# Kernel optimization log

Measured on AMD Instinct MI355X. Metric: run time of the kernel, lower is better.

## Reference

```python
import jax, jax.numpy as jnp
import numpy as np

INPUT_SIZE = 256
HIDDEN = 64
VOCAB = 8000
B, T = 64, 256


def _lstm_layer(x_seq, W_ih, W_hh, b_ih, b_hh):
    # x_seq: [B, T, D_in]; PyTorch gate order: i, f, g, o
    Bsz = x_seq.shape[0]
    H = W_hh.shape[1]
    # Precompute input projections for all timesteps (one big GEMM)
    x_proj = jnp.einsum('btd,gd->btg', x_seq, W_ih) + b_ih + b_hh  # [B,T,4H]

    def step(carry, xt):
        h, c = carry
        gates = xt + h @ W_hh.T  # [B,4H]
        i, f, g, o = jnp.split(gates, 4, axis=-1)
        i = jax.nn.sigmoid(i)
        f = jax.nn.sigmoid(f)
        g = jnp.tanh(g)
        o = jax.nn.sigmoid(o)
        c = f * c + i * g
        h = o * jnp.tanh(c)
        return (h, c), h

    zeros = jnp.zeros((Bsz, H), x_seq.dtype)
    _, hs = jax.lax.scan(step, (zeros, zeros), jnp.swapaxes(x_proj, 0, 1))
    return jnp.swapaxes(hs, 0, 1)  # [B,T,H]


def setup_inputs() -> dict:
    key = jax.random.key(0)
    ks = jax.random.split(key, 12)
    s0 = 1.0 / np.sqrt(HIDDEN)
    x = jax.random.normal(ks[0], (B, T, INPUT_SIZE), dtype=jnp.float32)
    W_ih0 = jax.random.uniform(ks[1], (4 * HIDDEN, INPUT_SIZE), jnp.float32, -s0, s0)
    W_hh0 = jax.random.uniform(ks[2], (4 * HIDDEN, HIDDEN), jnp.float32, -s0, s0)
    b_ih0 = jax.random.uniform(ks[3], (4 * HIDDEN,), jnp.float32, -s0, s0)
    b_hh0 = jax.random.uniform(ks[4], (4 * HIDDEN,), jnp.float32, -s0, s0)
    W_ih1 = jax.random.uniform(ks[5], (4 * HIDDEN, HIDDEN), jnp.float32, -s0, s0)
    W_hh1 = jax.random.uniform(ks[6], (4 * HIDDEN, HIDDEN), jnp.float32, -s0, s0)
    b_ih1 = jax.random.uniform(ks[7], (4 * HIDDEN,), jnp.float32, -s0, s0)
    b_hh1 = jax.random.uniform(ks[8], (4 * HIDDEN,), jnp.float32, -s0, s0)
    Wl = jax.random.uniform(ks[9], (VOCAB, HIDDEN), jnp.float32, -s0, s0)
    bl = jax.random.uniform(ks[10], (VOCAB,), jnp.float32, -s0, s0)
    return {"x": x, "W_ih0": W_ih0, "W_hh0": W_hh0, "b_ih0": b_ih0, "b_hh0": b_hh0,
            "W_ih1": W_ih1, "W_hh1": W_hh1, "b_ih1": b_ih1, "b_hh1": b_hh1,
            "Wl": Wl, "bl": bl}


def reference(x, W_ih0, W_hh0, b_ih0, b_hh0, W_ih1, W_hh1, b_ih1, b_hh1, Wl, bl):
    h1 = _lstm_layer(x, W_ih0, W_hh0, b_ih0, b_hh0)   # [B,T,H]
    h2 = _lstm_layer(h1, W_ih1, W_hh1, b_ih1, b_hh1)  # [B,T,H]
    return jnp.einsum('bth,vh->btv', h2, Wl) + bl      # [B,T,VOCAB]
```

## Files before the change

### kernel.cpp

```cpp
#include <hip/hip_runtime.h>
#include <math.h>

#define HID 64
#define G4 256
#define TSTEPS 256
#define BATCH 64
#define MTOT 16384
#define NVOCAB 8000

__device__ __forceinline__ float tanh_s(float x){
    float ax = fabsf(x);
    float e = __expf(-2.0f*ax);
    float t = (1.0f - e)/(1.0f + e);
    return x >= 0.f ? t : -t;
}

__global__ void transpose_k(const float* __restrict__ src, float* __restrict__ dst, int R, int C){
    int idx = blockIdx.x*256 + threadIdx.x;
    if (idx < R*C){
        int c = idx / R;
        int r = idx - c*R;
        dst[idx] = src[r*C + c];
    }
}

__global__ void bsum_k(const float* __restrict__ a, const float* __restrict__ b, float* __restrict__ o, int n){
    int i = blockIdx.x*256 + threadIdx.x;
    if (i < n) o[i] = a[i] + b[i];
}

template<int KTOT>
__global__ __launch_bounds__(256) void gemm_bias(
    const float* __restrict__ A, const float* __restrict__ Bt,
    const float* __restrict__ bias, float* __restrict__ C,
    int M, int N)
{
    __shared__ float As[128][65];
    __shared__ float Bs[64][128];
    const int tid = threadIdx.x;
    const int tx = tid & 15;
    const int ty = tid >> 4;
    const int m0 = blockIdx.y * 128;
    const int n0 = blockIdx.x * 128;

    float4 acc0[8], acc1[8];
    #pragma unroll
    for (int i = 0; i < 8; i++){
        acc0[i] = make_float4(0.f,0.f,0.f,0.f);
        acc1[i] = make_float4(0.f,0.f,0.f,0.f);
    }

    for (int k0 = 0; k0 < KTOT; k0 += 64){
        {
            const int mi_b = tid >> 4;
            const int k4   = (tid & 15) * 4;
            #pragma unroll
            for (int it = 0; it < 8; it++){
                int mi = it*16 + mi_b;
                float4 v = *(const float4*)(A + (size_t)(m0+mi)*KTOT + k0 + k4);
                As[mi][k4+0] = v.x; As[mi][k4+1] = v.y;
                As[mi][k4+2] = v.z; As[mi][k4+3] = v.w;
            }
        }
        {
            const int ki_b = tid >> 5;
            const int vj   = (tid & 31) * 4;
            #pragma unroll
            for (int it = 0; it < 8; it++){
                int ki = it*8 + ki_b;
                float4 v = make_float4(0.f,0.f,0.f,0.f);
                if (n0 + vj < N)
                    v = *(const float4*)(Bt + (size_t)(k0+ki)*N + n0 + vj);
                *(float4*)&Bs[ki][vj] = v;
            }
        }
        __syncthreads();

        #pragma unroll 8
        for (int k = 0; k < 64; k++){
            float4 b0 = *(const float4*)&Bs[k][tx*4];
            float4 b1 = *(const float4*)&Bs[k][64 + tx*4];
            #pragma unroll
            for (int i = 0; i < 8; i++){
                float av = As[ty*8+i][k];
                acc0[i].x = fmaf(av, b0.x, acc0[i].x);
                acc0[i].y = fmaf(av, b0.y, acc0[i].y);
                acc0[i].z = fmaf(av, b0.z, acc0[i].z);
                acc0[i].w = fmaf(av, b0.w, acc0[i].w);
                acc1[i].x = fmaf(av, b1.x, acc1[i].x);
                acc1[i].y = fmaf(av, b1.y, acc1[i].y);
                acc1[i].z = fmaf(av, b1.z, acc1[i].z);
                acc1[i].w = fmaf(av, b1.w, acc1[i].w);
            }
        }
        __syncthreads();
    }

    const int v0a = n0 + tx*4;
    const int v0b = n0 + 64 + tx*4;
    float4 ba = make_float4(0.f,0.f,0.f,0.f);
    float4 bb = make_float4(0.f,0.f,0.f,0.f);
    if (v0a < N) ba = *(const float4*)(bias + v0a);
    if (v0b < N) bb = *(const float4*)(bias + v0b);
    #pragma unroll
    for (int i = 0; i < 8; i++){
        int m = m0 + ty*8 + i;
        float* crow = C + (size_t)m*N;
        if (v0a < N){
            float4 r;
            r.x = acc0[i].x + ba.x; r.y = acc0[i].y + ba.y;
            r.z = acc0[i].z + ba.z; r.w = acc0[i].w + ba.w;
            *(float4*)(crow + v0a) = r;
        }
        if (v0b < N){
            float4 r;
            r.x = acc1[i].x + bb.x; r.y = acc1[i].y + bb.y;
            r.z = acc1[i].z + bb.z; r.w = acc1[i].w + bb.w;
            *(float4*)(crow + v0b) = r;
        }
    }
}

__global__ __launch_bounds__(256) void lstm_recur(
    const float* __restrict__ XP, const float* __restrict__ Whh,
    float* __restrict__ Hout)
{
    const int b = blockIdx.x;
    const int tid = threadIdx.x;
    __shared__ float4 hsh[16];
    __shared__ float gsh[256];

    float4 w[16];
    const float4* wr = (const float4*)(Whh + (size_t)tid*HID);
    #pragma unroll
    for (int i = 0; i < 16; i++) w[i] = wr[i];

    float c = 0.f;
    if (tid < 64) ((float*)hsh)[tid] = 0.f;
    __syncthreads();

    const float* xprow = XP + (size_t)b*TSTEPS*G4 + tid;
    const bool is_tanh = (tid >= 128) && (tid < 192);
    float xn = xprow[0];

    for (int t = 0; t < TSTEPS; t++){
        float a = xn;
        if (t+1 < TSTEPS) xn = xprow[(size_t)(t+1)*G4];

        float s0=0.f, s1=0.f, s2=0.f, s3=0.f;
        #pragma unroll
        for (int i = 0; i < 16; i += 4){
            float4 h0 = hsh[i+0];
            float4 h1 = hsh[i+1];
            float4 h2 = hsh[i+2];
            float4 h3 = hsh[i+3];
            s0 = fmaf(w[i+0].x,h0.x,s0); s0 = fmaf(w[i+0].y,h0.y,s0);
            s0 = fmaf(w[i+0].z,h0.z,s0); s0 = fmaf(w[i+0].w,h0.w,s0);
            s1 = fmaf(w[i+1].x,h1.x,s1); s1 = fmaf(w[i+1].y,h1.y,s1);
            s1 = fmaf(w[i+1].z,h1.z,s1); s1 = fmaf(w[i+1].w,h1.w,s1);
            s2 = fmaf(w[i+2].x,h2.x,s2); s2 = fmaf(w[i+2].y,h2.y,s2);
            s2 = fmaf(w[i+2].z,h2.z,s2); s2 = fmaf(w[i+2].w,h2.w,s2);
            s3 = fmaf(w[i+3].x,h3.x,s3); s3 = fmaf(w[i+3].y,h3.y,s3);
            s3 = fmaf(w[i+3].z,h3.z,s3); s3 = fmaf(w[i+3].w,h3.w,s3);
        }
        a += (s0+s1) + (s2+s3);

        float aa = is_tanh ? 2.f*a : a;
        float sg = 1.f/(1.f + __expf(-aa));
        float act = is_tanh ? 2.f*sg - 1.f : sg;
        gsh[tid] = act;
        __syncthreads();

        if (tid < 64){
            float ig = gsh[tid];
            float fg = gsh[64+tid];
            float gg = gsh[128+tid];
            float og = gsh[192+tid];
            c = fmaf(fg, c, ig*gg);
            float hn = og * tanh_s(c);
            ((float*)hsh)[tid] = hn;
            Hout[((size_t)b*TSTEPS + t)*HID + tid] = hn;
        }
        __syncthreads();
    }
}

extern "C" void kernel_launch(void* const* d_in, const int* in_sizes, int n_in,
                              void* d_out, int out_size, void* d_ws, size_t ws_size,
                              hipStream_t stream)
{
    const float* x    = (const float*)d_in[0];
    const float* Wih0 = (const float*)d_in[1];
    const float* Whh0 = (const float*)d_in[2];
    const float* bih0 = (const float*)d_in[3];
    const float* bhh0 = (const float*)d_in[4];
    const float* Wih1 = (const float*)d_in[5];
    const float* Whh1 = (const float*)d_in[6];
    const float* bih1 = (const float*)d_in[7];
    const float* bhh1 = (const float*)d_in[8];
    const float* Wl   = (const float*)d_in[9];
    const float* bl   = (const float*)d_in[10];
    float* out = (float*)d_out;

    float* ws  = (float*)d_ws;
    float* Wt0 = ws;
    float* Wt1 = Wt0 + 65536;
    float* WlT = Wt1 + 16384;
    float* bs0 = WlT + 512000;
    float* bs1 = bs0 + 256;
    float* xp0 = bs1 + 256;
    float* xp1 = xp0 + 4194304;
    float* h1  = xp1 + 4194304;
    float* h2  = h1  + 1048576;

    transpose_k<<<256, 256, 0, stream>>>(Wih0, Wt0, 256, 256);
    transpose_k<<<64,  256, 0, stream>>>(Wih1, Wt1, 256, 64);
    transpose_k<<<2000,256, 0, stream>>>(Wl,   WlT, 8000, 64);
    bsum_k<<<1, 256, 0, stream>>>(bih0, bhh0, bs0, 256);
    bsum_k<<<1, 256, 0, stream>>>(bih1, bhh1, bs1, 256);

    gemm_bias<256><<<dim3(2,128), 256, 0, stream>>>(x, Wt0, bs0, xp0, MTOT, 256);
    lstm_recur<<<BATCH, 256, 0, stream>>>(xp0, Whh0, h1);

    gemm_bias<64><<<dim3(2,128), 256, 0, stream>>>(h1, Wt1, bs1, xp1, MTOT, 256);
    lstm_recur<<<BATCH, 256, 0, stream>>>(xp1, Whh1, h2);

    gemm_bias<64><<<dim3(63,128), 256, 0, stream>>>(h2, WlT, bl, out, MTOT, NVOCAB);
}
```

Before: 1.038 ms.

## Drop weight transposes, use NT GEMM, and halve LSTM step barriers

The GEMM now reads weights in their original row-major [N,K] layout and transposes both A and B tiles into k-major shared memory, so the three transpose kernels go away and A values are read as float4. The LSTM recurrence interleaves the four gates of each hidden unit across adjacent lanes and gathers them with wave shuffles. This removes one of the two block barriers per timestep and the gate shared-memory round trip. Hidden states are kept in a full shared-memory history and written to global memory once at the end. Input projections are prefetched two steps ahead, at the cost of a large shared allocation per block.

```diff
diff --git a/kernel.cpp b/kernel.cpp
--- a/kernel.cpp
+++ b/kernel.cpp
@@ -15,28 +15,19 @@
     return x >= 0.f ? t : -t;
 }
 
-__global__ void transpose_k(const float* __restrict__ src, float* __restrict__ dst, int R, int C){
-    int idx = blockIdx.x*256 + threadIdx.x;
-    if (idx < R*C){
-        int c = idx / R;
-        int r = idx - c*R;
-        dst[idx] = src[r*C + c];
-    }
-}
-
 __global__ void bsum_k(const float* __restrict__ a, const float* __restrict__ b, float* __restrict__ o, int n){
     int i = blockIdx.x*256 + threadIdx.x;
     if (i < n) o[i] = a[i] + b[i];
 }
 
 template<int KTOT>
-__global__ __launch_bounds__(256) void gemm_bias(
-    const float* __restrict__ A, const float* __restrict__ Bt,
+__global__ __launch_bounds__(256, 2) void gemm_bias_nt(
+    const float* __restrict__ A, const float* __restrict__ B,
     const float* __restrict__ bias, float* __restrict__ C,
     int M, int N)
 {
-    __shared__ float As[128][65];
-    __shared__ float Bs[64][128];
+    __shared__ float As[64][132];
+    __shared__ float Bs[64][132];
     const int tid = threadIdx.x;
     const int tx = tid & 15;
     const int ty = tid >> 4;
@@ -50,47 +41,41 @@
         acc1[i] = make_float4(0.f,0.f,0.f,0.f);
     }
 
+    const int rl = tid & 15;
+    const int k4 = (tid >> 4) * 4;
+
     for (int k0 = 0; k0 < KTOT; k0 += 64){
-        {
-            const int mi_b = tid >> 4;
-            const int k4   = (tid & 15) * 4;
-            #pragma unroll
-            for (int it = 0; it < 8; it++){
-                int mi = it*16 + mi_b;
-                float4 v = *(const float4*)(A + (size_t)(m0+mi)*KTOT + k0 + k4);
-                As[mi][k4+0] = v.x; As[mi][k4+1] = v.y;
-                As[mi][k4+2] = v.z; As[mi][k4+3] = v.w;
-            }
-        }
-        {
-            const int ki_b = tid >> 5;
-            const int vj   = (tid & 31) * 4;
-            #pragma unroll
-            for (int it = 0; it < 8; it++){
-                int ki = it*8 + ki_b;
-                float4 v = make_float4(0.f,0.f,0.f,0.f);
-                if (n0 + vj < N)
-                    v = *(const float4*)(Bt + (size_t)(k0+ki)*N + n0 + vj);
-                *(float4*)&Bs[ki][vj] = v;
-            }
+        #pragma unroll
+        for (int it = 0; it < 8; it++){
+            int r = it*16 + rl;
+            float4 va = *(const float4*)(A + (size_t)(m0+r)*KTOT + k0 + k4);
+            As[k4+0][r] = va.x; As[k4+1][r] = va.y;
+            As[k4+2][r] = va.z; As[k4+3][r] = va.w;
+            float4 vb = make_float4(0.f,0.f,0.f,0.f);
+            if (n0 + r < N)
+                vb = *(const float4*)(B + (size_t)(n0+r)*KTOT + k0 + k4);
+            Bs[k4+0][r] = vb.x; Bs[k4+1][r] = vb.y;
+            Bs[k4+2][r] = vb.z; Bs[k4+3][r] = vb.w;
         }
         __syncthreads();
 
         #pragma unroll 8
         for (int k = 0; k < 64; k++){
+            float4 a0 = *(const float4*)&As[k][ty*8];
+            float4 a1 = *(const float4*)&As[k][ty*8 + 4];
             float4 b0 = *(const float4*)&Bs[k][tx*4];
             float4 b1 = *(const float4*)&Bs[k][64 + tx*4];
+            float av[8] = {a0.x,a0.y,a0.z,a0.w,a1.x,a1.y,a1.z,a1.w};
             #pragma unroll
             for (int i = 0; i < 8; i++){
-                float av = As[ty*8+i][k];
-                acc0[i].x = fmaf(av, b0.x, acc0[i].x);
-                acc0[i].y = fmaf(av, b0.y, acc0[i].y);
-                acc0[i].z = fmaf(av, b0.z, acc0[i].z);
-                acc0[i].w = fmaf(av, b0.w, acc0[i].w);
-                acc1[i].x = fmaf(av, b1.x, acc1[i].x);
-                acc1[i].y = fmaf(av, b1.y, acc1[i].y);
-                acc1[i].z = fmaf(av, b1.z, acc1[i].z);
-                acc1[i].w = fmaf(av, b1.w, acc1[i].w);
+                acc0[i].x = fmaf(av[i], b0.x, acc0[i].x);
+                acc0[i].y = fmaf(av[i], b0.y, acc0[i].y);
+                acc0[i].z = fmaf(av[i], b0.z, acc0[i].z);
+                acc0[i].w = fmaf(av[i], b0.w, acc0[i].w);
+                acc1[i].x = fmaf(av[i], b1.x, acc1[i].x);
+                acc1[i].y = fmaf(av[i], b1.y, acc1[i].y);
+                acc1[i].z = fmaf(av[i], b1.z, acc1[i].z);
+                acc1[i].w = fmaf(av[i], b1.w, acc1[i].w);
             }
         }
         __syncthreads();
@@ -127,33 +112,45 @@
 {
     const int b = blockIdx.x;
     const int tid = threadIdx.x;
-    __shared__ float4 hsh[16];
-    __shared__ float gsh[256];
+    const int lane = tid & 63;
+    const int wave = tid >> 6;
+    const int g  = lane & 3;
+    const int j  = wave*16 + (lane >> 2);
+    const int row = g*64 + j;
+    const bool gb0 = (g & 1) != 0;
+    const bool gb1 = (g & 2) != 0;
+    const bool is_g = (g == 2);
+
+    __shared__ __align__(16) float hist[TSTEPS+1][HID];
 
     float4 w[16];
-    const float4* wr = (const float4*)(Whh + (size_t)tid*HID);
-    #pragma unroll
-    for (int i = 0; i < 16; i++) w[i] = wr[i];
-
+    {
+        const float4* wr = (const float4*)(Whh + (size_t)row*HID);
+        #pragma unroll
+        for (int i = 0; i < 16; i++) w[i] = wr[i];
+    }
+
+    if (tid < HID) hist[0][tid] = 0.f;
+    __syncthreads();
+
+    const float* xprow = XP + (size_t)b*TSTEPS*G4 + row;
+    float xn0 = xprow[0];
+    float xn1 = xprow[G4];
     float c = 0.f;
-    if (tid < 64) ((float*)hsh)[tid] = 0.f;
-    __syncthreads();
-
-    const float* xprow = XP + (size_t)b*TSTEPS*G4 + tid;
-    const bool is_tanh = (tid >= 128) && (tid < 192);
-    float xn = xprow[0];
 
     for (int t = 0; t < TSTEPS; t++){
-        float a = xn;
-        if (t+1 < TSTEPS) xn = xprow[(size_t)(t+1)*G4];
-
+        float a = xn0;
+        xn0 = xn1;
+        if (t + 2 < TSTEPS) xn1 = xprow[(size_t)(t+2)*G4];
+
+        const float4* hv = (const float4*)hist[t];
         float s0=0.f, s1=0.f, s2=0.f, s3=0.f;
         #pragma unroll
         for (int i = 0; i < 16; i += 4){
-            float4 h0 = hsh[i+0];
-            float4 h1 = hsh[i+1];
-            float4 h2 = hsh[i+2];
-            float4 h3 = hsh[i+3];
+            float4 h0 = hv[i+0];
+            float4 h1 = hv[i+1];
+            float4 h2 = hv[i+2];
+            float4 h3 = hv[i+3];
             s0 = fmaf(w[i+0].x,h0.x,s0); s0 = fmaf(w[i+0].y,h0.y,s0);
             s0 = fmaf(w[i+0].z,h0.z,s0); s0 = fmaf(w[i+0].w,h0.w,s0);
             s1 = fmaf(w[i+1].x,h1.x,s1); s1 = fmaf(w[i+1].y,h1.y,s1);
@@ -165,24 +162,32 @@
         }
         a += (s0+s1) + (s2+s3);
 
-        float aa = is_tanh ? 2.f*a : a;
+        float aa = is_g ? 2.f*a : a;
         float sg = 1.f/(1.f + __expf(-aa));
-        float act = is_tanh ? 2.f*sg - 1.f : sg;
-        gsh[tid] = act;
+        float act = is_g ? 2.f*sg - 1.f : sg;
+
+        float a1v = __shfl_xor(act, 1, 64);
+        float a2v = __shfl_xor(act, 2, 64);
+        float a3v = __shfl_xor(act, 3, 64);
+        float x0 = gb0 ? a1v : act;
+        float x1 = gb0 ? act : a1v;
+        float x2 = gb0 ? a3v : a2v;
+        float x3 = gb0 ? a2v : a3v;
+        float ig = gb1 ? x2 : x0;
+        float fg = gb1 ? x3 : x1;
+        float gg = gb1 ? x0 : x2;
+        float og = gb1 ? x1 : x3;
+
+        c = fmaf(fg, c, ig*gg);
+        float hn = og * tanh_s(c);
+        if (g == 0) hist[t+1][j] = hn;
         __syncthreads();
-
-        if (tid < 64){
-            float ig = gsh[tid];
-            float fg = gsh[64+tid];
-            float gg = gsh[128+tid];
-            float og = gsh[192+tid];
-            c = fmaf(fg, c, ig*gg);
-            float hn = og * tanh_s(c);
-            ((float*)hsh)[tid] = hn;
-            Hout[((size_t)b*TSTEPS + t)*HID + tid] = hn;
-        }
-        __syncthreads();
-    }
+    }
+
+    const float4* h4 = (const float4*)&hist[1][0];
+    float4* o4 = (float4*)(Hout + (size_t)b*TSTEPS*HID);
+    #pragma unroll 4
+    for (int i = tid; i < TSTEPS*HID/4; i += 256) o4[i] = h4[i];
 }
 
 extern "C" void kernel_launch(void* const* d_in, const int* in_sizes, int n_in,
@@ -203,27 +208,21 @@
     float* out = (float*)d_out;
 
     float* ws  = (float*)d_ws;
-    float* Wt0 = ws;
-    float* Wt1 = Wt0 + 65536;
-    float* WlT = Wt1 + 16384;
-    float* bs0 = WlT + 512000;
+    float* bs0 = ws;
     float* bs1 = bs0 + 256;
     float* xp0 = bs1 + 256;
     float* xp1 = xp0 + 4194304;
     float* h1  = xp1 + 4194304;
     float* h2  = h1  + 1048576;
 
-    transpose_k<<<256, 256, 0, stream>>>(Wih0, Wt0, 256, 256);
-    transpose_k<<<64,  256, 0, stream>>>(Wih1, Wt1, 256, 64);
-    transpose_k<<<2000,256, 0, stream>>>(Wl,   WlT, 8000, 64);
     bsum_k<<<1, 256, 0, stream>>>(bih0, bhh0, bs0, 256);
     bsum_k<<<1, 256, 0, stream>>>(bih1, bhh1, bs1, 256);
 
-    gemm_bias<256><<<dim3(2,128), 256, 0, stream>>>(x, Wt0, bs0, xp0, MTOT, 256);
+    gemm_bias_nt<256><<<dim3(2,128), 256, 0, stream>>>(x, Wih0, bs0, xp0, MTOT, 256);
     lstm_recur<<<BATCH, 256, 0, stream>>>(xp0, Whh0, h1);
 
-    gemm_bias<64><<<dim3(2,128), 256, 0, stream>>>(h1, Wt1, bs1, xp1, MTOT, 256);
+    gemm_bias_nt<64><<<dim3(2,128), 256, 0, stream>>>(h1, Wih1, bs1, xp1, MTOT, 256);
     lstm_recur<<<BATCH, 256, 0, stream>>>(xp1, Whh1, h2);
 
-    gemm_bias<64><<<dim3(63,128), 256, 0, stream>>>(h2, WlT, bl, out, MTOT, NVOCAB);
-}
+    gemm_bias_nt<64><<<dim3(63,128), 256, 0, stream>>>(h2, Wl, bl, out, MTOT, NVOCAB);
+}
```

Result: faster. 1.012 ms (-2.5%).
